# Performance work log

Hardware: AMD Instinct MI355X
Metric: run time of the kernel (lower is better)

Reference implementation:

```python
import jax, jax.numpy as jnp
import numpy as np

EPS = 1e-10

def norm_t(x, axis):
    # zero-mean + L2 normalize along `axis` (standard NCC normalization)
    xc = x - jnp.mean(x, axis=axis, keepdims=True)
    return xc / (jnp.linalg.norm(xc, axis=axis, keepdims=True) + EPS)

def setup_inputs() -> dict:
    key = jax.random.key(0)
    k1, k2 = jax.random.split(key)
    input_compressed = jax.random.normal(k1, (1, 16, 131072), dtype=jnp.float32)  # [B, K, N]
    cmat = jax.random.normal(k2, (16, 1024), dtype=jnp.float32)                   # [K, D]
    return {"input_compressed": input_compressed, "cmat": cmat}

def reference(input_compressed, cmat):
    a = norm_t(input_compressed, axis=-2)          # [B, K, N], normalized over K
    b = norm_t(cmat, axis=0)                       # [K, D],    normalized over K
    ncc = jnp.einsum('bkn,kd->bnd', a, b)          # [B, N, D] correlation volume
    # torch: argmax(transpose(ncc,-2,-1), dim=-2) -> argmax over D -> [B, N]
    pred_depths = jnp.argmax(ncc, axis=-1)         # [B, N] int depth-bin indices
    return pred_depths
```

## Files before the change

### kernel.cpp

```cpp
#include <hip/hip_runtime.h>
#include <hip/hip_bf16.h>
#include <math.h>

#define N_PTS  131072
#define K_DIM  16
#define D_BINS 1024
#define MARGIN_P 3.5e-4f

typedef short bf16x8 __attribute__((ext_vector_type(8)));
typedef float f32x4  __attribute__((ext_vector_type(4)));

#define WS_OFF_BN  64
#define WS_OFF_B1  65600
#define WS_OFF_B2  98368
#define WS_NEED    131136

__device__ __forceinline__ void norm_np(const float* __restrict__ p,
                                        int stride, int n, float* __restrict__ a) {
#pragma clang fp contract(off)
    float v[K_DIM];
#pragma unroll
    for (int k = 0; k < K_DIM; ++k) v[k] = p[(size_t)k * stride + n];
    float s = v[0];
#pragma unroll
    for (int k = 1; k < K_DIM; ++k) s = s + v[k];
    const float mean = s / 16.0f;
    float sq[K_DIM];
#pragma unroll
    for (int k = 0; k < K_DIM; ++k) { a[k] = v[k] - mean; sq[k] = a[k] * a[k]; }
    float ss = sq[0];
#pragma unroll
    for (int k = 1; k < K_DIM; ++k) ss = ss + sq[k];
    const float denom = sqrtf(ss) + 1e-10f;
#pragma unroll
    for (int k = 0; k < K_DIM; ++k) a[k] = a[k] / denom;
}

__device__ __forceinline__ unsigned short bf16_bits(float f) {
    __hip_bfloat16 h = __float2bfloat16(f);
    unsigned short u;
    __builtin_memcpy(&u, &h, 2);
    return u;
}
__device__ __forceinline__ float bf16_val(float f) {
    return __bfloat162float(__float2bfloat16(f));
}

__device__ __forceinline__ unsigned v_med3u(unsigned a, unsigned b, unsigned c) {
    unsigned d;
    asm("v_med3_u32 %0, %1, %2, %3" : "=v"(d) : "v"(a), "v"(b), "v"(c));
    return d;
}

__global__ __launch_bounds__(256) void prep_b(
    const float* __restrict__ cmat, float* __restrict__ bnT,
    unsigned short* __restrict__ B1, unsigned short* __restrict__ B2) {
#pragma clang fp contract(off)
    const int d = blockIdx.x * 256 + threadIdx.x;
    if (d >= D_BINS) return;

    float t[K_DIM];
    norm_np(cmat, D_BINS, d, t);

    const int tile = d >> 4, n = d & 15;
#pragma unroll
    for (int k = 0; k < K_DIM; ++k) {
        bnT[d * K_DIM + k] = t[k];
        const float hi_f = bf16_val(t[k]);
        const int idx = tile * 256 + ((k >> 3) * 16 + n) * 8 + (k & 7);
        B1[idx] = bf16_bits(t[k]);
        B2[idx] = bf16_bits(t[k] - hi_f);
    }
}

__global__ __launch_bounds__(512, 8) void mfma_screen(
    const float* __restrict__ x, const uint4* __restrict__ B1frag,
    const uint4* __restrict__ B2frag,
    const float* __restrict__ bnT, int* __restrict__ out) {
#pragma clang fp contract(off)
    __shared__ uint4 ldsB[2048];

    {
#pragma unroll
        for (int j = 0; j < 4; ++j)
            ldsB[threadIdx.x + j * 512] = B1frag[threadIdx.x + j * 512];
    }

    const int lane = threadIdx.x & 63;
    const int wv   = threadIdx.x >> 6;
    const int W    = blockIdx.x * 8 + wv;
    const int P    = W * 16;
    const int m    = lane & 15;
    const int q    = lane >> 4;

    bf16x8 A, A2;
    {
        float a[K_DIM];
        norm_np(x, N_PTS, P + m, a);
        unsigned short els[8];
#pragma unroll
        for (int j = 0; j < 8; ++j) {
            const int k = (q & 1) * 8 + j;
            if (q < 2) els[j] = bf16_bits(a[k]);
            else       els[j] = bf16_bits(a[k] - bf16_val(a[k]));
        }
        __builtin_memcpy(&A, els, 16);
        A2 = (q < 2) ? A : (bf16x8)(short)0;
    }

    __syncthreads();

    const uint4* b1p = ldsB + (lane & 31);
    const uint4* b2p = B2frag + (lane & 31);

    unsigned ub1[4], ub2[4];
#pragma unroll
    for (int r = 0; r < 4; ++r) { ub1[r] = 0u; ub2[r] = 0u; }

    const unsigned mask  = 0xFFFFFC00u;
    const unsigned dbase = 1023u - (unsigned)m;

#pragma unroll 4
    for (int i = 0; i < 64; ++i) {
        const uint4 w1 = b1p[i * 32];
        const uint4 w2 = b2p[i * 32];
        const bf16x8 bf1 = __builtin_bit_cast(bf16x8, w1);
        const bf16x8 bf2 = __builtin_bit_cast(bf16x8, w2);

        f32x4 acc = __builtin_amdgcn_mfma_f32_16x16x32_bf16(
            A, bf1, (f32x4){2.f, 2.f, 2.f, 2.f}, 0, 0, 0);
        acc = __builtin_amdgcn_mfma_f32_16x16x32_bf16(A2, bf2, acc, 0, 0, 0);

        const unsigned dcomp = dbase - (unsigned)(i * 16);
#pragma unroll
        for (int r = 0; r < 4; ++r) {
            const unsigned u   = (__float_as_uint(acc[r]) & mask) | dcomp;
            const unsigned nb2 = v_med3u(ub1[r], ub2[r], u);
            ub1[r] = max(ub1[r], u);
            ub2[r] = nb2;
        }
    }

    unsigned fail16 = 0;
#pragma unroll
    for (int r = 0; r < 4; ++r) {
        unsigned u1 = ub1[r], u2 = ub2[r];
#pragma unroll
        for (int s = 1; s <= 8; s <<= 1) {
            const unsigned o1 = (unsigned)__shfl_xor((int)u1, s, 16);
            const unsigned o2 = (unsigned)__shfl_xor((int)u2, s, 16);
            const unsigned n1 = max(u1, o1);
            u2 = max(min(u1, o1), max(u2, o2));
            u1 = n1;
        }
        int fail = 0;
        if (m == 0) {
            const int p  = P + q * 4 + r;
            const float s1 = __uint_as_float(u1 & mask);
            const float s2 = __uint_as_float(u2 & mask);
            if (s1 - s2 > MARGIN_P) out[p] = 1023 - (int)(u1 & 1023u);
            else fail = 1;
        }
        const unsigned long long bm = __ballot(fail);
        fail16 |= (unsigned)((bm      ) & 1ull) << (r);
        fail16 |= (unsigned)((bm >> 16) & 1ull) << (4 + r);
        fail16 |= (unsigned)((bm >> 32) & 1ull) << (8 + r);
        fail16 |= (unsigned)((bm >> 48) & 1ull) << (12 + r);
    }

    __syncthreads();
    int* pool = reinterpret_cast<int*>(ldsB);
    if (threadIdx.x == 0) pool[0] = 0;
    __syncthreads();
    if (lane == 0) {
        unsigned f = fail16;
        while (f) {
            const int s = __builtin_ffs((int)f) - 1;
            f &= f - 1;
            const int pos = atomicAdd(pool, 1);
            pool[1 + pos] = P + s;
        }
    }
    __syncthreads();
    const int cnt = pool[0];

    for (int j = wv; j < cnt; j += 8) {
        const int p = pool[1 + j];

        float a[K_DIM];
        norm_np(x, N_PTS, p, a);

        float best = -3.402823466e38f;
        int   idx  = 0x7fffffff;
        const float4* b4 = (const float4*)bnT;
#pragma unroll 4
        for (int t = 0; t < 16; ++t) {
            const int d = t * 64 + lane;
            const float4 q0 = b4[d * 4 + 0];
            const float4 q1 = b4[d * 4 + 1];
            const float4 q2 = b4[d * 4 + 2];
            const float4 q3 = b4[d * 4 + 3];
            float sc;
            sc = a[0] * q0.x;
            sc = sc + a[1]  * q0.y; sc = sc + a[2]  * q0.z; sc = sc + a[3]  * q0.w;
            sc = sc + a[4]  * q1.x; sc = sc + a[5]  * q1.y; sc = sc + a[6]  * q1.z;
            sc = sc + a[7]  * q1.w; sc = sc + a[8]  * q2.x; sc = sc + a[9]  * q2.y;
            sc = sc + a[10] * q2.z; sc = sc + a[11] * q2.w; sc = sc + a[12] * q3.x;
            sc = sc + a[13] * q3.y; sc = sc + a[14] * q3.z; sc = sc + a[15] * q3.w;
            if (sc > best) { best = sc; idx = d; }
        }
#pragma unroll
        for (int mk = 1; mk <= 32; mk <<= 1) {
            const float ob = __shfl_xor(best, mk);
            const int   oi = __shfl_xor(idx,  mk);
            if (ob > best || (ob == best && oi < idx)) { best = ob; idx = oi; }
        }
        if (lane == 0) out[p] = idx;
    }
}

__global__ __launch_bounds__(256) void ncc_argmax_np32(
    const float* __restrict__ x, const float* __restrict__ bnT,
    int* __restrict__ out) {
#pragma clang fp contract(off)
    const int n = blockIdx.x * 256 + threadIdx.x;
    float a[K_DIM];
    norm_np(x, N_PTS, n, a);

    float best = -3.402823466e38f;
    int   idx  = 0;
    const float4* b4 = (const float4*)bnT;
#pragma unroll 2
    for (int d = 0; d < D_BINS; ++d) {
        const float4 q0 = b4[d * 4 + 0];
        const float4 q1 = b4[d * 4 + 1];
        const float4 q2 = b4[d * 4 + 2];
        const float4 q3 = b4[d * 4 + 3];
        float sc;
        sc = a[0] * q0.x;
        sc = sc + a[1]  * q0.y; sc = sc + a[2]  * q0.z; sc = sc + a[3]  * q0.w;
        sc = sc + a[4]  * q1.x; sc = sc + a[5]  * q1.y; sc = sc + a[6]  * q1.z;
        sc = sc + a[7]  * q1.w; sc = sc + a[8]  * q2.x; sc = sc + a[9]  * q2.y;
        sc = sc + a[10] * q2.z; sc = sc + a[11] * q2.w; sc = sc + a[12] * q3.x;
        sc = sc + a[13] * q3.y; sc = sc + a[14] * q3.z; sc = sc + a[15] * q3.w;
        if (sc > best) { best = sc; idx = d; }
    }
    out[n] = idx;
}

__global__ __launch_bounds__(256) void normalize_rows_only(
    const float* __restrict__ cmat, float* __restrict__ bnT) {
#pragma clang fp contract(off)
    const int d = blockIdx.x * 256 + threadIdx.x;
    if (d >= D_BINS) return;
    float t[K_DIM];
    norm_np(cmat, D_BINS, d, t);
#pragma unroll
    for (int k = 0; k < K_DIM; ++k) bnT[d * K_DIM + k] = t[k];
}

extern "C" void kernel_launch(void* const* d_in, const int* in_sizes, int n_in,
                              void* d_out, int out_size, void* d_ws, size_t ws_size,
                              hipStream_t stream) {
    const float* x    = (const float*)d_in[0];
    const float* cmat = (const float*)d_in[1];
    int* out = (int*)d_out;
    char* ws = (char*)d_ws;

    if (ws_size >= (size_t)WS_NEED) {
        float*          bnT = (float*)(ws + WS_OFF_BN);
        unsigned short* B1  = (unsigned short*)(ws + WS_OFF_B1);
        unsigned short* B2  = (unsigned short*)(ws + WS_OFF_B2);

        prep_b<<<4, 256, 0, stream>>>(cmat, bnT, B1, B2);
        mfma_screen<<<1024, 512, 0, stream>>>(
            x, (const uint4*)(ws + WS_OFF_B1), (const uint4*)(ws + WS_OFF_B2),
            bnT, out);
    } else {
        float* bnT = (float*)(ws + WS_OFF_BN);
        normalize_rows_only<<<4, 256, 0, stream>>>(cmat, bnT);
        ncc_argmax_np32<<<512, 256, 0, stream>>>(x, bnT, out);
    }
}
```

Before: 99.73 us.

## Process two 16-point tiles per wave to reuse B fragments

Each wave now normalizes and screens 32 points instead of 16. It issues two sets of MFMAs per loaded B1/B2 fragment, so each LDS and global B load is shared by twice as many points. The launch grid is halved and launch bounds are relaxed to allow more registers for the doubled accumulators and top-2 trackers. The low-part MFMA now multiplies the full A operand with B2 instead of zeroing the lo lanes. That adds one small extra term while keeping the same MFMA count. The trade-off is fewer resident waves per CU and higher register pressure, which may reduce latency hiding.

```diff
diff --git a/kernel.cpp b/kernel.cpp
--- a/kernel.cpp
+++ b/kernel.cpp
@@ -73,7 +73,7 @@
     }
 }
 
-__global__ __launch_bounds__(512, 8) void mfma_screen(
+__global__ __launch_bounds__(512, 4) void mfma_screen(
     const float* __restrict__ x, const uint4* __restrict__ B1frag,
     const uint4* __restrict__ B2frag,
     const float* __restrict__ bnT, int* __restrict__ out) {
@@ -89,23 +89,32 @@
     const int lane = threadIdx.x & 63;
     const int wv   = threadIdx.x >> 6;
     const int W    = blockIdx.x * 8 + wv;
-    const int P    = W * 16;
+    const int P    = W * 32;
     const int m    = lane & 15;
     const int q    = lane >> 4;
 
-    bf16x8 A, A2;
+    bf16x8 Ae, Ao;
     {
         float a[K_DIM];
+        unsigned short els[8];
+
         norm_np(x, N_PTS, P + m, a);
-        unsigned short els[8];
 #pragma unroll
         for (int j = 0; j < 8; ++j) {
             const int k = (q & 1) * 8 + j;
             if (q < 2) els[j] = bf16_bits(a[k]);
             else       els[j] = bf16_bits(a[k] - bf16_val(a[k]));
         }
-        __builtin_memcpy(&A, els, 16);
-        A2 = (q < 2) ? A : (bf16x8)(short)0;
+        __builtin_memcpy(&Ae, els, 16);
+
+        norm_np(x, N_PTS, P + 16 + m, a);
+#pragma unroll
+        for (int j = 0; j < 8; ++j) {
+            const int k = (q & 1) * 8 + j;
+            if (q < 2) els[j] = bf16_bits(a[k]);
+            else       els[j] = bf16_bits(a[k] - bf16_val(a[k]));
+        }
+        __builtin_memcpy(&Ao, els, 16);
     }
 
     __syncthreads();
@@ -113,12 +122,15 @@
     const uint4* b1p = ldsB + (lane & 31);
     const uint4* b2p = B2frag + (lane & 31);
 
-    unsigned ub1[4], ub2[4];
-#pragma unroll
-    for (int r = 0; r < 4; ++r) { ub1[r] = 0u; ub2[r] = 0u; }
+    unsigned ub1e[4], ub2e[4], ub1o[4], ub2o[4];
+#pragma unroll
+    for (int r = 0; r < 4; ++r) {
+        ub1e[r] = 0u; ub2e[r] = 0u; ub1o[r] = 0u; ub2o[r] = 0u;
+    }
 
     const unsigned mask  = 0xFFFFFC00u;
     const unsigned dbase = 1023u - (unsigned)m;
+    const f32x4 cb = {2.f, 2.f, 2.f, 2.f};
 
 #pragma unroll 4
     for (int i = 0; i < 64; ++i) {
@@ -127,45 +139,55 @@
         const bf16x8 bf1 = __builtin_bit_cast(bf16x8, w1);
         const bf16x8 bf2 = __builtin_bit_cast(bf16x8, w2);
 
-        f32x4 acc = __builtin_amdgcn_mfma_f32_16x16x32_bf16(
-            A, bf1, (f32x4){2.f, 2.f, 2.f, 2.f}, 0, 0, 0);
-        acc = __builtin_amdgcn_mfma_f32_16x16x32_bf16(A2, bf2, acc, 0, 0, 0);
+        f32x4 ae = __builtin_amdgcn_mfma_f32_16x16x32_bf16(Ae, bf1, cb, 0, 0, 0);
+        ae = __builtin_amdgcn_mfma_f32_16x16x32_bf16(Ae, bf2, ae, 0, 0, 0);
+        f32x4 ao = __builtin_amdgcn_mfma_f32_16x16x32_bf16(Ao, bf1, cb, 0, 0, 0);
+        ao = __builtin_amdgcn_mfma_f32_16x16x32_bf16(Ao, bf2, ao, 0, 0, 0);
 
         const unsigned dcomp = dbase - (unsigned)(i * 16);
 #pragma unroll
         for (int r = 0; r < 4; ++r) {
-            const unsigned u   = (__float_as_uint(acc[r]) & mask) | dcomp;
-            const unsigned nb2 = v_med3u(ub1[r], ub2[r], u);
-            ub1[r] = max(ub1[r], u);
-            ub2[r] = nb2;
-        }
-    }
-
-    unsigned fail16 = 0;
-#pragma unroll
-    for (int r = 0; r < 4; ++r) {
-        unsigned u1 = ub1[r], u2 = ub2[r];
-#pragma unroll
-        for (int s = 1; s <= 8; s <<= 1) {
-            const unsigned o1 = (unsigned)__shfl_xor((int)u1, s, 16);
-            const unsigned o2 = (unsigned)__shfl_xor((int)u2, s, 16);
-            const unsigned n1 = max(u1, o1);
-            u2 = max(min(u1, o1), max(u2, o2));
-            u1 = n1;
-        }
-        int fail = 0;
-        if (m == 0) {
-            const int p  = P + q * 4 + r;
-            const float s1 = __uint_as_float(u1 & mask);
-            const float s2 = __uint_as_float(u2 & mask);
-            if (s1 - s2 > MARGIN_P) out[p] = 1023 - (int)(u1 & 1023u);
-            else fail = 1;
-        }
-        const unsigned long long bm = __ballot(fail);
-        fail16 |= (unsigned)((bm      ) & 1ull) << (r);
-        fail16 |= (unsigned)((bm >> 16) & 1ull) << (4 + r);
-        fail16 |= (unsigned)((bm >> 32) & 1ull) << (8 + r);
-        fail16 |= (unsigned)((bm >> 48) & 1ull) << (12 + r);
+            const unsigned ue  = (__float_as_uint(ae[r]) & mask) | dcomp;
+            const unsigned n2e = v_med3u(ub1e[r], ub2e[r], ue);
+            ub1e[r] = max(ub1e[r], ue);
+            ub2e[r] = n2e;
+            const unsigned uo  = (__float_as_uint(ao[r]) & mask) | dcomp;
+            const unsigned n2o = v_med3u(ub1o[r], ub2o[r], uo);
+            ub1o[r] = max(ub1o[r], uo);
+            ub2o[r] = n2o;
+        }
+    }
+
+    unsigned fail32 = 0;
+#pragma unroll
+    for (int g = 0; g < 2; ++g) {
+#pragma unroll
+        for (int r = 0; r < 4; ++r) {
+            unsigned u1 = g ? ub1o[r] : ub1e[r];
+            unsigned u2 = g ? ub2o[r] : ub2e[r];
+#pragma unroll
+            for (int s = 1; s <= 8; s <<= 1) {
+                const unsigned o1 = (unsigned)__shfl_xor((int)u1, s, 16);
+                const unsigned o2 = (unsigned)__shfl_xor((int)u2, s, 16);
+                const unsigned n1 = max(u1, o1);
+                u2 = max(min(u1, o1), max(u2, o2));
+                u1 = n1;
+            }
+            int fail = 0;
+            if (m == 0) {
+                const int p  = P + g * 16 + q * 4 + r;
+                const float s1 = __uint_as_float(u1 & mask);
+                const float s2 = __uint_as_float(u2 & mask);
+                if (s1 - s2 > MARGIN_P) out[p] = 1023 - (int)(u1 & 1023u);
+                else fail = 1;
+            }
+            const unsigned long long bm = __ballot(fail);
+            const int base = g * 16 + r;
+            fail32 |= (unsigned)((bm      ) & 1ull) << (base);
+            fail32 |= (unsigned)((bm >> 16) & 1ull) << (base + 4);
+            fail32 |= (unsigned)((bm >> 32) & 1ull) << (base + 8);
+            fail32 |= (unsigned)((bm >> 48) & 1ull) << (base + 12);
+        }
     }
 
     __syncthreads();
@@ -173,7 +195,7 @@
     if (threadIdx.x == 0) pool[0] = 0;
     __syncthreads();
     if (lane == 0) {
-        unsigned f = fail16;
+        unsigned f = fail32;
         while (f) {
             const int s = __builtin_ffs((int)f) - 1;
             f &= f - 1;
@@ -273,7 +295,7 @@
         unsigned short* B2  = (unsigned short*)(ws + WS_OFF_B2);
 
         prep_b<<<4, 256, 0, stream>>>(cmat, bnT, B1, B2);
-        mfma_screen<<<1024, 512, 0, stream>>>(
+        mfma_screen<<<512, 512, 0, stream>>>(
             x, (const uint4*)(ws + WS_OFF_B1), (const uint4*)(ws + WS_OFF_B2),
             bnT, out);
     } else {
```

Result: no change. 100.3 us (+0.5%).
